# Kernel tuning notes

Hardware: AMD Instinct MI355X
Metric: run time of the kernel (lower is better)

The kernel has to match this reference:

```python
import jax, jax.numpy as jnp
import numpy as np


def _shift_kernels():
    # [4,1,3,3] OIHW: left, right, up, down shift-difference kernels (as in torch module)
    kl = [[0, 0, 0], [-1, 1, 0], [0, 0, 0]]
    kr = [[0, 0, 0], [0, 1, -1], [0, 0, 0]]
    ku = [[0, -1, 0], [0, 1, 0], [0, 0, 0]]
    kd = [[0, 0, 0], [0, 1, 0], [0, -1, 0]]
    return jnp.asarray(np.stack([kl, kr, ku, kd])[:, None], dtype=jnp.float32)


def _avgpool4(x):
    # x: [B,1,H,W] -> [B,1,H//4,W//4], non-overlapping 4x4 mean (nn.AvgPool2d(4))
    b, c, h, w = x.shape
    return x.reshape(b, c, h // 4, 4, w // 4, 4).mean(axis=(3, 5))


def setup_inputs() -> dict:
    key = jax.random.key(0)
    k1, k2 = jax.random.split(key)
    org = jax.random.uniform(k1, (32, 3, 512, 512), dtype=jnp.float32)
    enhance = jax.random.uniform(k2, (32, 3, 512, 512), dtype=jnp.float32)
    return {"org": org, "enhance": enhance}


def reference(org, enhance):
    org_pool = _avgpool4(jnp.mean(org, axis=1, keepdims=True))
    enh_pool = _avgpool4(jnp.mean(enhance, axis=1, keepdims=True))
    # conv is linear, so D_org_k - D_enh_k == conv(org_pool - enh_pool, k).
    diff = org_pool - enh_pool  # [B,1,h,w]
    d = jax.lax.conv_general_dilated(
        diff, _shift_kernels(), window_strides=(1, 1),
        padding=((1, 1), (1, 1)),
        dimension_numbers=("NCHW", "OIHW", "NCHW"))  # [B,4,h,w]
    # torch: mean(D_left + D_right + D_up + D_down) over [B,1,h,w]
    return jnp.mean(jnp.sum(d * d, axis=1))
```

## Files before the change

### kernel.cpp

```cpp
#include <hip/hip_runtime.h>

#define NB 32
#define PH 128
#define PW 128
#define NPOOL  (NB * PH * PW)
#define NBLK   (NPOOL / 256)
#define INV48  (1.0f / 48.0f)

typedef float vf4 __attribute__((ext_vector_type(4)));

__global__ __launch_bounds__(256) void pool_fused_kernel(
    const vf4* __restrict__ o4, const vf4* __restrict__ e4,
    float* __restrict__ pooled, float* __restrict__ out)
{
    if (blockIdx.x == 0 && threadIdx.x == 0) out[0] = 0.f;

    int idx = blockIdx.x * 256 + threadIdx.x;
    int x = idx & (PW - 1);
    int y = (idx >> 7) & (PH - 1);
    int b = idx >> 14;

    int rbase = ((b * 3) * 512 + (y << 2)) * 128 + x;

    vf4 ov[12], ev[12];
#pragma unroll
    for (int i = 0; i < 12; ++i) {
        int c = i >> 2, dy = i & 3;
        int a = rbase + (c * 512 + dy) * 128;
        ov[i] = __builtin_nontemporal_load(o4 + a);
        ev[i] = __builtin_nontemporal_load(e4 + a);
    }

    vf4 d = {0.f, 0.f, 0.f, 0.f};
#pragma unroll
    for (int i = 0; i < 12; ++i)
        d += ov[i] - ev[i];

    pooled[idx] = ((d.x + d.y) + (d.z + d.w)) * INV48;
}

__global__ __launch_bounds__(256) void spa_reduce_kernel(
    const float* __restrict__ pooled, float* __restrict__ out)
{
    int idx = blockIdx.x * 256 + threadIdx.x;
    int x = idx & (PW - 1);
    int y = (idx >> 7) & (PH - 1);
    const float* p = pooled + (idx >> 14) * (PH * PW);

    float c  = p[y * PW + x];
    float l  = (x > 0)      ? p[y * PW + x - 1] : 0.f;
    float r  = (x < PW - 1) ? p[y * PW + x + 1] : 0.f;
    float u  = (y > 0)      ? p[(y - 1) * PW + x] : 0.f;
    float dn = (y < PH - 1) ? p[(y + 1) * PW + x] : 0.f;

    float dl = c - l, dr = c - r, du = c - u, dd = c - dn;
    float s = (dl * dl + dr * dr) + (du * du + dd * dd);

#pragma unroll
    for (int off = 32; off > 0; off >>= 1)
        s += __shfl_down(s, off, 64);

    __shared__ float smem[4];
    int lane = threadIdx.x & 63;
    int wid  = threadIdx.x >> 6;
    if (lane == 0) smem[wid] = s;
    __syncthreads();
    if (threadIdx.x == 0)
        atomicAdd(out, ((smem[0] + smem[1]) + (smem[2] + smem[3]))
                           * (1.0f / (float)NPOOL));
}

extern "C" void kernel_launch(void* const* d_in, const int* in_sizes, int n_in,
                              void* d_out, int out_size, void* d_ws, size_t ws_size,
                              hipStream_t stream) {
    const vf4* o4 = (const vf4*)d_in[0];
    const vf4* e4 = (const vf4*)d_in[1];
    float* out    = (float*)d_out;
    float* pooled = (float*)d_ws;

    pool_fused_kernel<<<NBLK, 256, 0, stream>>>(o4, e4, pooled, out);
    spa_reduce_kernel<<<NBLK, 256, 0, stream>>>(pooled, out);
}
```

Before: 219.4 us.

## Split pooling per channel plane with contiguous loads and LDS row reduce

Result: slower. 236.5 us (+7.8%).

```diff
diff --git a/kernel.cpp b/kernel.cpp
--- a/kernel.cpp
+++ b/kernel.cpp
@@ -1,59 +1,79 @@
 #include <hip/hip_runtime.h>
 
-#define NB 32
 #define PH 128
 #define PW 128
-#define NPOOL  (NB * PH * PW)
-#define NBLK   (NPOOL / 256)
-#define INV48  (1.0f / 48.0f)
+#define NPOOL   (32 * PH * PW)
+#define NPLANE  96
+#define PLANE_F4 65536
+#define ROWS_PB 8
+#define RG_PER_PLANE 64
+#define NBLK_A  (NPLANE * RG_PER_PLANE)
+#define NBLK_B  (NPOOL / 256)
+#define INV48   (1.0f / 48.0f)
 
 typedef float vf4 __attribute__((ext_vector_type(4)));
 
-__global__ __launch_bounds__(256) void pool_fused_kernel(
+__device__ __forceinline__ float hsum(vf4 d) {
+    return (d.x + d.y) + (d.z + d.w);
+}
+
+__global__ __launch_bounds__(256) void stageA_pool_kernel(
     const vf4* __restrict__ o4, const vf4* __restrict__ e4,
-    float* __restrict__ pooled, float* __restrict__ out)
+    float* __restrict__ partial, float* __restrict__ out)
 {
     if (blockIdx.x == 0 && threadIdx.x == 0) out[0] = 0.f;
 
-    int idx = blockIdx.x * 256 + threadIdx.x;
-    int x = idx & (PW - 1);
-    int y = (idx >> 7) & (PH - 1);
-    int b = idx >> 14;
+    const int t  = threadIdx.x;
+    const int p  = blockIdx.x >> 6;
+    const int rg = blockIdx.x & 63;
+    const int base = p * PLANE_F4 + rg * (ROWS_PB * 128);
 
-    int rbase = ((b * 3) * 512 + (y << 2)) * 128 + x;
+    vf4 o0 = o4[base +         t];
+    vf4 o1 = o4[base + 256  +  t];
+    vf4 o2 = o4[base + 512  +  t];
+    vf4 o3 = o4[base + 768  +  t];
+    vf4 e0 = e4[base +         t];
+    vf4 e1 = e4[base + 256  +  t];
+    vf4 e2 = e4[base + 512  +  t];
+    vf4 e3 = e4[base + 768  +  t];
 
-    vf4 ov[12], ev[12];
-#pragma unroll
-    for (int i = 0; i < 12; ++i) {
-        int c = i >> 2, dy = i & 3;
-        int a = rbase + (c * 512 + dy) * 128;
-        ov[i] = __builtin_nontemporal_load(o4 + a);
-        ev[i] = __builtin_nontemporal_load(e4 + a);
-    }
+    __shared__ float lds[ROWS_PB][128];
+    const int r0 = t >> 7;
+    const int c  = t & 127;
+    lds[r0 + 0][c] = hsum(o0 - e0);
+    lds[r0 + 2][c] = hsum(o1 - e1);
+    lds[r0 + 4][c] = hsum(o2 - e2);
+    lds[r0 + 6][c] = hsum(o3 - e3);
+    __syncthreads();
 
-    vf4 d = {0.f, 0.f, 0.f, 0.f};
-#pragma unroll
-    for (int i = 0; i < 12; ++i)
-        d += ov[i] - ev[i];
-
-    pooled[idx] = ((d.x + d.y) + (d.z + d.w)) * INV48;
+    const int yp = t >> 7;
+    const int x  = t & 127;
+    float v = (lds[4 * yp + 0][x] + lds[4 * yp + 1][x])
+            + (lds[4 * yp + 2][x] + lds[4 * yp + 3][x]);
+    partial[p * (PH * PW) + (rg * 2 + yp) * PW + x] = v * INV48;
 }
 
 __global__ __launch_bounds__(256) void spa_reduce_kernel(
-    const float* __restrict__ pooled, float* __restrict__ out)
+    const float* __restrict__ partial, float* __restrict__ out)
 {
     int idx = blockIdx.x * 256 + threadIdx.x;
-    int x = idx & (PW - 1);
-    int y = (idx >> 7) & (PH - 1);
-    const float* p = pooled + (idx >> 14) * (PH * PW);
+    int pw = idx & (PW - 1);
+    int ph = (idx >> 7) & (PH - 1);
+    int b  = idx >> 14;
 
-    float c  = p[y * PW + x];
-    float l  = (x > 0)      ? p[y * PW + x - 1] : 0.f;
-    float r  = (x < PW - 1) ? p[y * PW + x + 1] : 0.f;
-    float u  = (y > 0)      ? p[(y - 1) * PW + x] : 0.f;
-    float dn = (y < PH - 1) ? p[(y + 1) * PW + x] : 0.f;
+    const float* p0 = partial + (b * 3 + 0) * (PH * PW);
+    const float* p1 = partial + (b * 3 + 1) * (PH * PW);
+    const float* p2 = partial + (b * 3 + 2) * (PH * PW);
 
-    float dl = c - l, dr = c - r, du = c - u, dd = c - dn;
+    #define POOLED(y, x) (p0[(y) * PW + (x)] + p1[(y) * PW + (x)] + p2[(y) * PW + (x)])
+    float cc = POOLED(ph, pw);
+    float l  = (pw > 0)      ? POOLED(ph, pw - 1) : 0.f;
+    float r  = (pw < PW - 1) ? POOLED(ph, pw + 1) : 0.f;
+    float u  = (ph > 0)      ? POOLED(ph - 1, pw) : 0.f;
+    float d  = (ph < PH - 1) ? POOLED(ph + 1, pw) : 0.f;
+    #undef POOLED
+
+    float dl = cc - l, dr = cc - r, du = cc - u, dd = cc - d;
     float s = (dl * dl + dr * dr) + (du * du + dd * dd);
 
 #pragma unroll
@@ -75,9 +95,9 @@
                               hipStream_t stream) {
     const vf4* o4 = (const vf4*)d_in[0];
     const vf4* e4 = (const vf4*)d_in[1];
-    float* out    = (float*)d_out;
-    float* pooled = (float*)d_ws;
+    float* out     = (float*)d_out;
+    float* partial = (float*)d_ws;
 
-    pool_fused_kernel<<<NBLK, 256, 0, stream>>>(o4, e4, pooled, out);
-    spa_reduce_kernel<<<NBLK, 256, 0, stream>>>(pooled, out);
+    stageA_pool_kernel<<<NBLK_A, 256, 0, stream>>>(o4, e4, partial, out);
+    spa_reduce_kernel<<<NBLK_B, 256, 0, stream>>>(partial, out);
 }
```
